# Kernel tuning notes

Measured on AMD Instinct MI355X. Metric: run time of the kernel, lower is better.

The kernel has to match this reference:

```python
import jax, jax.numpy as jnp
import numpy as np

N, E, G = 100000, 1600000, 256
F_IN, HID, NCLS = 16, 64, 2
EPS = 1e-5


def segment_mean(v, seg, num_segments):
    s = jax.ops.segment_sum(v, seg, num_segments=num_segments)
    c = jax.ops.segment_sum(jnp.ones((v.shape[0], 1), v.dtype), seg, num_segments=num_segments)
    return s / jnp.maximum(c, 1.0)


def graph_norm(x, seg, weight, bias, mean_scale):
    # PyG GraphNorm: per-graph mean/var with learnable mean_scale
    mean = segment_mean(x, seg, G)                      # [G, C]
    centered = x - mean_scale * mean[seg]               # [N, C]
    var = segment_mean(centered * centered, seg, G)     # [G, C]
    return weight * centered * jax.lax.rsqrt(var[seg] + EPS) + bias


def gcn_conv(x, W, b, row, col, n):
    # PyG GCNConv: h = x @ W; symmetric norm with added self-loops; scatter-add; + bias
    h = x @ W                                           # [N, C_out]
    deg = jnp.zeros((n,), x.dtype).at[row].add(1.0) + 1.0  # +1 self-loop
    dinv = jax.lax.rsqrt(deg)
    norm = (dinv[row] * dinv[col])[:, None]             # [E, 1]
    agg = jnp.zeros_like(h).at[row].add(norm * h[col])  # neighbor messages
    agg = agg + (dinv * dinv)[:, None] * h              # self-loop messages
    return agg + b


def setup_inputs():
    key = jax.random.key(0)
    ks = jax.random.split(key, 16)
    x = jax.random.normal(ks[0], (N, F_IN), jnp.float32)
    edge_index = jax.random.randint(ks[1], (2, E), 0, N, jnp.int32)
    batch = jnp.sort(jax.random.randint(ks[2], (N,), 0, G, jnp.int32))
    s = lambda k, shp: jax.random.normal(k, shp, jnp.float32) * 0.05
    return {
        "x": x, "edge_index": edge_index, "batch": batch,
        "gn0_w": jnp.ones((F_IN,)), "gn0_b": jnp.zeros((F_IN,)), "gn0_ms": jnp.ones((F_IN,)),
        "W1": s(ks[3], (F_IN, HID)), "b1": jnp.zeros((HID,)),
        "gn1_w": jnp.ones((HID,)), "gn1_b": jnp.zeros((HID,)), "gn1_ms": jnp.ones((HID,)),
        "W2": s(ks[4], (HID, HID)), "b2": jnp.zeros((HID,)),
        "gn2_w": jnp.ones((HID,)), "gn2_b": jnp.zeros((HID,)), "gn2_ms": jnp.ones((HID,)),
        "W3": s(ks[5], (HID, HID)), "b3": jnp.zeros((HID,)),
        "Wd": s(ks[6], (HID, HID)), "bd": jnp.zeros((HID,)),
        "Wo": s(ks[7], (HID, NCLS)), "bo": jnp.zeros((NCLS,)),
    }


def reference(x, edge_index, batch, gn0_w, gn0_b, gn0_ms, W1, b1, gn1_w, gn1_b, gn1_ms,
              W2, b2, gn2_w, gn2_b, gn2_ms, W3, b3, Wd, bd, Wo, bo):
    row, col = edge_index[0], edge_index[1]
    h = graph_norm(x, batch, gn0_w, gn0_b, gn0_ms)
    h = jax.nn.relu(gcn_conv(h, W1, b1, row, col, N))
    h = graph_norm(h, batch, gn1_w, gn1_b, gn1_ms)
    h = jax.nn.relu(gcn_conv(h, W2, b2, row, col, N))
    h = graph_norm(h, batch, gn2_w, gn2_b, gn2_ms)
    h = jax.nn.relu(gcn_conv(h, W3, b3, row, col, N))
    g = segment_mean(h, batch, G)                       # global_mean_pool -> [G, HID]
    # dropout is identity in eval mode
    g = jax.nn.relu(g @ Wd + bd)
    logits = g @ Wo + bo
    return jax.nn.softmax(logits, axis=1)
```

## Files before the change

### kernel.cpp

```cpp
#include <hip/hip_runtime.h>
#include <hip/hip_bf16.h>

#define NN 100000
#define NE 1600000
#define NG 256
#define FIN 16
#define HID 64
#define NBK 391
#define NTILE 391
#define PMAX 4864

__device__ __forceinline__ int lower_bound_i(const int* __restrict__ b, int n, int v) {
    int lo = 0, hi = n;
    while (lo < hi) { int m = (lo + hi) >> 1; if (b[m] < v) lo = m + 1; else hi = m; }
    return lo;
}

__device__ __forceinline__ unsigned pack_bf16(float a, float b) {
    unsigned ua = __float_as_uint(a), ub = __float_as_uint(b);
    ua = (ua + 0x7fffu + ((ua >> 16) & 1u)) >> 16;
    ub = (ub + 0x7fffu + ((ub >> 16) & 1u)) & 0xffff0000u;
    return ua | ub;
}
#define BF_LO(u) __uint_as_float((u) << 16)
#define BF_HI(u) __uint_as_float((u) & 0xffff0000u)

__global__ __launch_bounds__(512) void k_zb(int* __restrict__ bhist) {
    bhist[threadIdx.x] = 0;
}

__global__ __launch_bounds__(512) void k_bhist(const int4* __restrict__ row4, int* __restrict__ bhist) {
    __shared__ int h[NBK];
    for (int i = threadIdx.x; i < NBK; i += 512) h[i] = 0;
    __syncthreads();
    int t0 = blockIdx.x * 1024 + threadIdx.x;
#pragma unroll
    for (int it = 0; it < 2; ++it) {
        int t = t0 + it * 512;
        if (t < NE / 4) {
            int4 r = row4[t];
            atomicAdd(&h[r.x >> 8], 1); atomicAdd(&h[r.y >> 8], 1);
            atomicAdd(&h[r.z >> 8], 1); atomicAdd(&h[r.w >> 8], 1);
        }
    }
    __syncthreads();
    for (int i = threadIdx.x; i < NBK; i += 512)
        if (h[i]) atomicAdd(&bhist[i], h[i]);
}

__global__ __launch_bounds__(512) void k_bscan(const int* __restrict__ bhist, int* __restrict__ bbase,
                                               int* __restrict__ bcur) {
    __shared__ int sc[512];
    int t = threadIdx.x;
    int v = (t < NBK) ? bhist[t] : 0;
    sc[t] = v;
    __syncthreads();
    int acc = v;
    for (int off = 1; off < 512; off <<= 1) {
        int add = (t >= off) ? sc[t - off] : 0;
        __syncthreads();
        acc += add;
        sc[t] = acc;
        __syncthreads();
    }
    if (t < NBK) { bbase[t] = acc - v; bcur[t] = acc - v; }
    if (t == NBK - 1) bbase[NBK] = acc;
}

__global__ __launch_bounds__(512) void k_bscatter(const int4* __restrict__ row4, const int4* __restrict__ col4,
                                                  int* __restrict__ bcur, int2* __restrict__ pairs) {
    __shared__ int lh[NBK], lofs[NBK], lbase[NBK], lc[NBK];
    __shared__ int sc[512];
    __shared__ int2 stg[4096];
    for (int i = threadIdx.x; i < NBK; i += 512) { lh[i] = 0; lc[i] = 0; }
    __syncthreads();
    int t0 = blockIdx.x * 1024 + threadIdx.x;
#pragma unroll
    for (int it = 0; it < 2; ++it) {
        int t = t0 + it * 512;
        if (t < NE / 4) {
            int4 r = row4[t];
            atomicAdd(&lh[r.x >> 8], 1); atomicAdd(&lh[r.y >> 8], 1);
            atomicAdd(&lh[r.z >> 8], 1); atomicAdd(&lh[r.w >> 8], 1);
        }
    }
    __syncthreads();
    {
        int t = threadIdx.x;
        int v = (t < NBK) ? lh[t] : 0;
        sc[t] = v;
        __syncthreads();
        int acc = v;
        for (int off = 1; off < 512; off <<= 1) {
            int add = (t >= off) ? sc[t - off] : 0;
            __syncthreads();
            acc += add;
            sc[t] = acc;
            __syncthreads();
        }
        if (t < NBK) lofs[t] = acc - v;
    }
    if (threadIdx.x < NBK) {
        int c = lh[threadIdx.x];
        lbase[threadIdx.x] = c ? atomicAdd(&bcur[threadIdx.x], c) : 0;
    }
    __syncthreads();
#pragma unroll
    for (int it = 0; it < 2; ++it) {
        int t = t0 + it * 512;
        if (t < NE / 4) {
            int4 r = row4[t];
            int4 c = col4[t];
            int b, rk;
            b = r.x >> 8; rk = atomicAdd(&lc[b], 1); stg[lofs[b] + rk] = make_int2(r.x, c.x);
            b = r.y >> 8; rk = atomicAdd(&lc[b], 1); stg[lofs[b] + rk] = make_int2(r.y, c.y);
            b = r.z >> 8; rk = atomicAdd(&lc[b], 1); stg[lofs[b] + rk] = make_int2(r.z, c.z);
            b = r.w >> 8; rk = atomicAdd(&lc[b], 1); stg[lofs[b] + rk] = make_int2(r.w, c.w);
        }
    }
    __syncthreads();
    int nv = min(4096, NE - blockIdx.x * 4096);
    for (int j = threadIdx.x; j < nv; j += 512) {
        int2 p = stg[j];
        int b = p.x >> 8;
        pairs[lbase[b] + (j - lofs[b])] = p;
    }
}

__global__ __launch_bounds__(256) void k_bsort(const int2* __restrict__ pairs, const int* __restrict__ bbase,
                                               int* __restrict__ csr_col, int* __restrict__ startv,
                                               int* __restrict__ degc, float* __restrict__ dinv) {
    __shared__ int2 prs[PMAX];
    __shared__ int colo[PMAX];
    __shared__ int cnt[256], ofs[256], c2[256], sc[256];
    int b = blockIdx.x;
    int s = bbase[b];
    int n = min(bbase[b + 1] - s, PMAX);
    cnt[threadIdx.x] = 0;
    c2[threadIdx.x] = 0;
    __syncthreads();
    for (int i = threadIdx.x; i < n; i += 256) {
        int2 p = pairs[s + i];
        prs[i] = p;
        atomicAdd(&cnt[p.x & 255], 1);
    }
    __syncthreads();
    {
        int t = threadIdx.x, v = cnt[t];
        sc[t] = v;
        __syncthreads();
        int acc = v;
        for (int off = 1; off < 256; off <<= 1) {
            int add = (t >= off) ? sc[t - off] : 0;
            __syncthreads();
            acc += add;
            sc[t] = acc;
            __syncthreads();
        }
        ofs[t] = acc - v;
    }
    __syncthreads();
    for (int i = threadIdx.x; i < n; i += 256) {
        int2 p = prs[i];
        int lr = p.x & 255;
        int rk = atomicAdd(&c2[lr], 1);
        colo[ofs[lr] + rk] = p.y;
    }
    __syncthreads();
    for (int i = threadIdx.x; i < n; i += 256) csr_col[s + i] = colo[i];
    int r = (b << 8) + threadIdx.x;
    if (r < NN) {
        int c = cnt[threadIdx.x];
        startv[r] = s + ofs[threadIdx.x];
        degc[r] = c;
        dinv[r] = rsqrtf((float)(c + 1));
    }
}

__global__ __launch_bounds__(256) void k_graphnorm16(const float* __restrict__ x, const int* __restrict__ batch,
                              const float* __restrict__ w, const float* __restrict__ b,
                              const float* __restrict__ ms, const float* __restrict__ dinv,
                              unsigned* __restrict__ xb) {
    constexpr int C = FIN, NPB = 256 / C;
    __shared__ float red[NPB][C], red2[NPB][C];
    __shared__ float mm_s[C], rs_s[C];
    int g = blockIdx.x;
    int s = lower_bound_i(batch, NN, g);
    int e = lower_bound_i(batch, NN, g + 1);
    float fc = (float)max(e - s, 1);
    int c = threadIdx.x % C, slot = threadIdx.x / C;

    float a1 = 0.f, a2 = 0.f;
    for (int i = s + slot; i < e; i += NPB) { float v = x[i * C + c]; a1 += v; a2 += v * v; }
    red[slot][c] = a1;
    red2[slot][c] = a2;
    __syncthreads();
    if (threadIdx.x < C) {
        float t1 = 0.f, t2 = 0.f;
        for (int k = 0; k < NPB; k++) { t1 += red[k][threadIdx.x]; t2 += red2[k][threadIdx.x]; }
        float mean = t1 / fc;
        float mm = ms[threadIdx.x] * mean;
        float var = t2 / fc - 2.f * mm * mean + mm * mm;
        mm_s[threadIdx.x] = mm;
        rs_s[threadIdx.x] = rsqrtf(var + 1e-5f);
    }
    __syncthreads();
    float mm = mm_s[c], ww = w[c] * rs_s[c], bb = b[c];
    for (int i = s + slot; i < e; i += NPB) {
        float v = (ww * (x[i * C + c] - mm) + bb) * dinv[i];
        float partner = __shfl_xor(v, 1);
        if ((c & 1) == 0) xb[(long)i * 8 + (c >> 1)] = pack_bf16(v, partner);
    }
}

__global__ __launch_bounds__(256) void k_gnstats(const float* __restrict__ x, const int* __restrict__ batch,
                          const float* __restrict__ w, const float* __restrict__ b,
                          const float* __restrict__ ms,
                          float* __restrict__ tabA, float* __restrict__ tabB) {
    constexpr int C = 64, NPB = 4;
    __shared__ float red[NPB][C], red2[NPB][C];
    int g = blockIdx.x;
    int s = lower_bound_i(batch, NN, g);
    int e = lower_bound_i(batch, NN, g + 1);
    float fc = (float)max(e - s, 1);
    int c = threadIdx.x & 63, slot = threadIdx.x >> 6;

    float a1 = 0.f, a2 = 0.f;
    for (int i = s + slot; i < e; i += NPB) { float v = x[i * C + c]; a1 += v; a2 += v * v; }
    red[slot][c] = a1;
    red2[slot][c] = a2;
    __syncthreads();
    if (threadIdx.x < C) {
        float t1 = 0.f, t2 = 0.f;
        for (int k = 0; k < NPB; k++) { t1 += red[k][threadIdx.x]; t2 += red2[k][threadIdx.x]; }
        float mean = t1 / fc;
        float mm = ms[threadIdx.x] * mean;
        float var = t2 / fc - 2.f * mm * mean + mm * mm;
        float A = w[threadIdx.x] * rsqrtf(var + 1e-5f);
        tabA[g * C + threadIdx.x] = A;
        tabB[g * C + threadIdx.x] = b[threadIdx.x] - A * mm;
    }
}

__global__ __launch_bounds__(256) void k_gg16(const unsigned* __restrict__ xb, const int* __restrict__ startv,
                        const int* __restrict__ degc, const float* __restrict__ dinv,
                        const int* __restrict__ csr_col, const float* __restrict__ W,
                        const float* __restrict__ bias, float* __restrict__ out) {
    __shared__ float Ws[FIN * 64];
    for (int i = threadIdx.x; i < FIN * 64; i += 256) Ws[i] = W[i];
    __syncthreads();
    int wave = (blockIdx.x * blockDim.x + threadIdx.x) >> 6;
    if (wave >= NN) return;
    int lane = threadIdx.x & 63;
    int p = lane & 7, g = lane >> 3;
    int s = startv[wave], cnt = degc[wave];
    float di = dinv[wave];
    float ax = 0.f, ay = 0.f;
    int k = g;
    for (; k + 8 < cnt; k += 16) {
        int c0 = csr_col[s + k], c1 = csr_col[s + k + 8];
        unsigned u0 = xb[(long)c0 * 8 + p], u1 = xb[(long)c1 * 8 + p];
        ax += BF_LO(u0) + BF_LO(u1);
        ay += BF_HI(u0) + BF_HI(u1);
    }
    for (; k < cnt; k += 8) {
        int c0 = csr_col[s + k];
        unsigned u0 = xb[(long)c0 * 8 + p];
        ax += BF_LO(u0);
        ay += BF_HI(u0);
    }
    ax += __shfl_xor(ax, 8);  ay += __shfl_xor(ay, 8);
    ax += __shfl_xor(ax, 16); ay += __shfl_xor(ay, 16);
    ax += __shfl_xor(ax, 32); ay += __shfl_xor(ay, 32);
    if (g == 0) {
        unsigned u = xb[(long)wave * 8 + p];
        ax = (ax + BF_LO(u)) * di;
        ay = (ay + BF_HI(u)) * di;
    }
    int j = lane;
    float acc = bias[j];
#pragma unroll
    for (int kk = 0; kk < 8; kk++) {
        float vx = __shfl(ax, kk);
        float vy = __shfl(ay, kk);
        acc += vx * Ws[(2 * kk) * 64 + j] + vy * Ws[(2 * kk + 1) * 64 + j];
    }
    out[(long)wave * 64 + j] = fmaxf(acc, 0.f);
}

__global__ __launch_bounds__(256) void k_gather64(const unsigned* __restrict__ h2, const int* __restrict__ startv,
                           const int* __restrict__ degc, const float* __restrict__ dinv,
                           const int* __restrict__ csr_col, const float* __restrict__ bias,
                           float* __restrict__ out) {
    int wave = (blockIdx.x * blockDim.x + threadIdx.x) >> 6;
    if (wave >= NN) return;
    int lane = threadIdx.x & 63;
    int p = lane & 31, g = lane >> 5;
    int s = startv[wave], cnt = degc[wave];
    float di = dinv[wave];
    float ax = 0.f, ay = 0.f;
    if (g == 0) {
        unsigned u = h2[(long)wave * 32 + p];
        ax = BF_LO(u);
        ay = BF_HI(u);
    }
    int k = g;
    for (; k + 6 < cnt; k += 8) {
        int c0 = csr_col[s + k], c1 = csr_col[s + k + 2],
            c2 = csr_col[s + k + 4], c3 = csr_col[s + k + 6];
        unsigned u0 = h2[(long)c0 * 32 + p], u1 = h2[(long)c1 * 32 + p],
                 u2 = h2[(long)c2 * 32 + p], u3 = h2[(long)c3 * 32 + p];
        ax += BF_LO(u0) + BF_LO(u1) + BF_LO(u2) + BF_LO(u3);
        ay += BF_HI(u0) + BF_HI(u1) + BF_HI(u2) + BF_HI(u3);
    }
    for (; k < cnt; k += 2) {
        int c0 = csr_col[s + k];
        unsigned u0 = h2[(long)c0 * 32 + p];
        ax += BF_LO(u0);
        ay += BF_HI(u0);
    }
    ax += __shfl_xor(ax, 32);
    ay += __shfl_xor(ay, 32);
    if (g == 0) {
        float2 r;
        r.x = fmaxf(ax * di + bias[2 * p], 0.f);
        r.y = fmaxf(ay * di + bias[2 * p + 1], 0.f);
        ((float2*)out)[(long)wave * 32 + p] = r;
    }
}

__global__ __launch_bounds__(256) void k_gemm64n(const float* __restrict__ x, const int* __restrict__ batch,
                          const float* __restrict__ tabA, const float* __restrict__ tabB,
                          const float* __restrict__ W, const float* __restrict__ dinv,
                          unsigned* __restrict__ h2) {
    constexpr int NPB = 100;
    __shared__ float xs[NPB * 64];
    __shared__ int gb[NPB];
    int base = blockIdx.x * NPB;
    int j = threadIdx.x & 63;
    float w[64];
#pragma unroll
    for (int k = 0; k < 64; k++) w[k] = W[k * 64 + j];
    for (int i = threadIdx.x; i < NPB; i += 256) gb[i] = batch[base + i];
    __syncthreads();
    for (int i = threadIdx.x; i < NPB * 64; i += 256) {
        int node = i >> 6, c = i & 63;
        int g2 = gb[node];
        xs[i] = tabA[g2 * 64 + c] * x[(long)(base + node) * 64 + c] + tabB[g2 * 64 + c];
    }
    __syncthreads();
    int s0 = threadIdx.x >> 6;
    for (int r = 0; r < 25; r++) {
        int sl = s0 * 25 + r;
        const float4* xv = (const float4*)&xs[sl * 64];
        float acc = 0.f;
#pragma unroll
        for (int k4 = 0; k4 < 16; k4++) {
            float4 v = xv[k4];
            acc += v.x * w[4 * k4] + v.y * w[4 * k4 + 1] + v.z * w[4 * k4 + 2] + v.w * w[4 * k4 + 3];
        }
        acc *= dinv[base + sl];
        float part = __shfl_xor(acc, 1);
        if ((j & 1) == 0) h2[(long)(base + sl) * 32 + (j >> 1)] = pack_bf16(acc, part);
    }
}

__global__ __launch_bounds__(1024) void k_pool(const float* __restrict__ x, const int* __restrict__ batch,
                       float* __restrict__ gpool) {
    __shared__ float red[16][64];
    int g = blockIdx.x;
    int s = lower_bound_i(batch, NN, g);
    int e = lower_bound_i(batch, NN, g + 1);
    int c = threadIdx.x & 63, slot = threadIdx.x >> 6;
    float acc = 0.f;
    for (int i = s + slot; i < e; i += 16) acc += x[i * 64 + c];
    red[slot][c] = acc;
    __syncthreads();
    if (threadIdx.x < 64) {
        float t = 0.f;
        for (int k = 0; k < 16; k++) t += red[k][threadIdx.x];
        gpool[g * 64 + threadIdx.x] = t / (float)max(e - s, 1);
    }
}

__global__ __launch_bounds__(64) void k_head(const float* __restrict__ gpool, const float* __restrict__ Wd,
                       const float* __restrict__ bd, const float* __restrict__ Wo,
                       const float* __restrict__ bo, float* __restrict__ out) {
    int g = blockIdx.x, j = threadIdx.x;
    __shared__ float gs[64];
    gs[j] = gpool[g * 64 + j];
    __syncthreads();
    float acc = bd[j];
    for (int k = 0; k < 64; k++) acc += gs[k] * Wd[k * 64 + j];
    float hv = fmaxf(acc, 0.f);
    float p0 = hv * Wo[j * 2 + 0], p1 = hv * Wo[j * 2 + 1];
    for (int off = 32; off; off >>= 1) { p0 += __shfl_down(p0, off); p1 += __shfl_down(p1, off); }
    if (j == 0) {
        float l0 = p0 + bo[0], l1 = p1 + bo[1];
        float m = fmaxf(l0, l1);
        float e0 = expf(l0 - m), e1 = expf(l1 - m);
        float inv = 1.f / (e0 + e1);
        out[g * 2 + 0] = e0 * inv;
        out[g * 2 + 1] = e1 * inv;
    }
}

extern "C" void kernel_launch(void* const* d_in, const int* in_sizes, int n_in,
                              void* d_out, int out_size, void* d_ws, size_t ws_size,
                              hipStream_t stream) {
    const float* x = (const float*)d_in[0];
    const int* ei = (const int*)d_in[1];
    const int* row = ei;
    const int* col = ei + NE;
    const int* batch = (const int*)d_in[2];
    const float* gn0w = (const float*)d_in[3];
    const float* gn0b = (const float*)d_in[4];
    const float* gn0ms = (const float*)d_in[5];
    const float* W1 = (const float*)d_in[6];
    const float* b1 = (const float*)d_in[7];
    const float* gn1w = (const float*)d_in[8];
    const float* gn1b = (const float*)d_in[9];
    const float* gn1ms = (const float*)d_in[10];
    const float* W2 = (const float*)d_in[11];
    const float* b2 = (const float*)d_in[12];
    const float* gn2w = (const float*)d_in[13];
    const float* gn2b = (const float*)d_in[14];
    const float* gn2ms = (const float*)d_in[15];
    const float* W3 = (const float*)d_in[16];
    const float* b3 = (const float*)d_in[17];
    const float* Wd = (const float*)d_in[18];
    const float* bd = (const float*)d_in[19];
    const float* Wo = (const float*)d_in[20];
    const float* bo = (const float*)d_in[21];
    float* outp = (float*)d_out;

    int* bhist = (int*)d_ws;
    int* bbase = bhist + 512;
    int* bcur = bbase + 512;
    int* startv = bcur + 512;
    int* degc = startv + NN;
    float* dinv = (float*)(degc + NN);
    int* csr_col = (int*)(dinv + NN);
    float* bufA = (float*)(csr_col + NE);
    float* bufB = bufA + (long)NN * HID;
    unsigned* h2 = (unsigned*)(bufB + (long)NN * HID);
    unsigned* xb = h2 + (long)NN * 32;
    float* tabA = (float*)(xb + (long)NN * 8);
    float* tabB = tabA + NG * HID;
    float* gpool = tabB + NG * HID;
    int2* pairs = (int2*)bufA;

    k_zb<<<1, 512, 0, stream>>>(bhist);
    k_bhist<<<NTILE, 512, 0, stream>>>((const int4*)row, bhist);
    k_bscan<<<1, 512, 0, stream>>>(bhist, bbase, bcur);
    k_bscatter<<<NTILE, 512, 0, stream>>>((const int4*)row, (const int4*)col, bcur, pairs);
    k_bsort<<<NBK, 256, 0, stream>>>(pairs, bbase, csr_col, startv, degc, dinv);

    k_graphnorm16<<<NG, 256, 0, stream>>>(x, batch, gn0w, gn0b, gn0ms, dinv, xb);
    k_gg16<<<(NN * 64 + 255) / 256, 256, 0, stream>>>(xb, startv, degc, dinv, csr_col, W1, b1, bufA);

    k_gnstats<<<NG, 256, 0, stream>>>(bufA, batch, gn1w, gn1b, gn1ms, tabA, tabB);
    k_gemm64n<<<NN / 100, 256, 0, stream>>>(bufA, batch, tabA, tabB, W2, dinv, h2);
    k_gather64<<<(NN * 64 + 255) / 256, 256, 0, stream>>>(h2, startv, degc, dinv, csr_col, b2, bufB);

    k_gnstats<<<NG, 256, 0, stream>>>(bufB, batch, gn2w, gn2b, gn2ms, tabA, tabB);
    k_gemm64n<<<NN / 100, 256, 0, stream>>>(bufB, batch, tabA, tabB, W3, dinv, h2);
    k_gather64<<<(NN * 64 + 255) / 256, 256, 0, stream>>>(h2, startv, degc, dinv, csr_col, b3, bufA);

    k_pool<<<NG, 1024, 0, stream>>>(bufA, batch, gpool);
    k_head<<<NG, 64, 0, stream>>>(gpool, Wd, bd, Wo, bo, outp);
}
```

Before: 454.9 us.

## Use bf16 MFMA GEMMs with per-graph folded GraphNorm weights and bf16 activations

Replaces the scalar FP32 node GEMMs with bf16 MFMA 16x16x32 kernels that run over per-graph 16-node tiles built by a new tiling kernel. GraphNorm scale and shift are folded into a per-graph weight matrix and bias, computed in the stats kernel. The first layer is split into a 16-wide gather and a separate MFMA GEMM. Intermediate activations are stored as bf16 instead of fp32 to cut memory traffic. In exchange it adds precision loss from bf16 weights and activations, extra launches, and padding waste on partial tiles.

```diff
diff --git a/kernel.cpp b/kernel.cpp
--- a/kernel.cpp
+++ b/kernel.cpp
@@ -9,6 +9,7 @@
 #define NBK 391
 #define NTILE 391
 #define PMAX 4864
+#define MAXT (NN / 16 + NG)
 
 __device__ __forceinline__ int lower_bound_i(const int* __restrict__ b, int n, int v) {
     int lo = 0, hi = n;
@@ -24,6 +25,10 @@
 }
 #define BF_LO(u) __uint_as_float((u) << 16)
 #define BF_HI(u) __uint_as_float((u) & 0xffff0000u)
+
+typedef __attribute__((ext_vector_type(8))) short bf16x8;
+typedef __attribute__((ext_vector_type(4))) float f32x4;
+union FU { uint4 u; bf16x8 v; };
 
 __global__ __launch_bounds__(512) void k_zb(int* __restrict__ bhist) {
     bhist[threadIdx.x] = 0;
@@ -177,6 +182,49 @@
     }
 }
 
+__global__ __launch_bounds__(256) void k_tiles(const int* __restrict__ batch, int* __restrict__ ntot,
+                                               int* __restrict__ tg, int* __restrict__ tbase,
+                                               int* __restrict__ tcnt) {
+    __shared__ int gst[NG + 1];
+    __shared__ int sc[NG];
+    int t = threadIdx.x;
+    gst[t] = lower_bound_i(batch, NN, t);
+    if (t == 0) gst[NG] = NN;
+    __syncthreads();
+    int ng = gst[t + 1] - gst[t];
+    int nt = (ng + 15) >> 4;
+    sc[t] = nt;
+    __syncthreads();
+    int acc = nt;
+    for (int off = 1; off < NG; off <<= 1) {
+        int add = (t >= off) ? sc[t - off] : 0;
+        __syncthreads();
+        acc += add;
+        sc[t] = acc;
+        __syncthreads();
+    }
+    int ofs = acc - nt;
+    for (int i = 0; i < nt; i++) {
+        tg[ofs + i] = t;
+        tbase[ofs + i] = gst[t] + i * 16;
+        tcnt[ofs + i] = min(16, ng - i * 16);
+    }
+    if (t == NG - 1) ntot[0] = acc;
+}
+
+__global__ __launch_bounds__(256) void k_prepw1(const float* __restrict__ W1, unsigned* __restrict__ Wt1p) {
+    int t = threadIdx.x;
+    int j = t >> 2, kq = t & 3;
+#pragma unroll
+    for (int i = 0; i < 4; i++) {
+        int idx = kq * 4 + i;
+        int k = idx * 2;
+        unsigned v = 0;
+        if (k < FIN) v = pack_bf16(W1[k * 64 + j], W1[(k + 1) * 64 + j]);
+        Wt1p[j * 16 + idx] = v;
+    }
+}
+
 __global__ __launch_bounds__(256) void k_graphnorm16(const float* __restrict__ x, const int* __restrict__ batch,
                               const float* __restrict__ w, const float* __restrict__ b,
                               const float* __restrict__ ms, const float* __restrict__ dinv,
@@ -213,12 +261,13 @@
     }
 }
 
-__global__ __launch_bounds__(256) void k_gnstats(const float* __restrict__ x, const int* __restrict__ batch,
+__global__ __launch_bounds__(256) void k_gnstats2(const unsigned* __restrict__ xw, const int* __restrict__ batch,
                           const float* __restrict__ w, const float* __restrict__ b,
-                          const float* __restrict__ ms,
-                          float* __restrict__ tabA, float* __restrict__ tabB) {
+                          const float* __restrict__ ms, const float* __restrict__ W,
+                          unsigned* __restrict__ Wtp, float* __restrict__ bias2) {
     constexpr int C = 64, NPB = 4;
     __shared__ float red[NPB][C], red2[NPB][C];
+    __shared__ float sA[C], sB[C];
     int g = blockIdx.x;
     int s = lower_bound_i(batch, NN, g);
     int e = lower_bound_i(batch, NN, g + 1);
@@ -226,7 +275,11 @@
     int c = threadIdx.x & 63, slot = threadIdx.x >> 6;
 
     float a1 = 0.f, a2 = 0.f;
-    for (int i = s + slot; i < e; i += NPB) { float v = x[i * C + c]; a1 += v; a2 += v * v; }
+    for (int i = s + slot; i < e; i += NPB) {
+        unsigned u = xw[(long)i * 32 + (c >> 1)];
+        float v = (c & 1) ? BF_HI(u) : BF_LO(u);
+        a1 += v; a2 += v * v;
+    }
     red[slot][c] = a1;
     red2[slot][c] = a2;
     __syncthreads();
@@ -237,18 +290,28 @@
         float mm = ms[threadIdx.x] * mean;
         float var = t2 / fc - 2.f * mm * mean + mm * mm;
         float A = w[threadIdx.x] * rsqrtf(var + 1e-5f);
-        tabA[g * C + threadIdx.x] = A;
-        tabB[g * C + threadIdx.x] = b[threadIdx.x] - A * mm;
-    }
-}
-
-__global__ __launch_bounds__(256) void k_gg16(const unsigned* __restrict__ xb, const int* __restrict__ startv,
-                        const int* __restrict__ degc, const float* __restrict__ dinv,
-                        const int* __restrict__ csr_col, const float* __restrict__ W,
-                        const float* __restrict__ bias, float* __restrict__ out) {
-    __shared__ float Ws[FIN * 64];
-    for (int i = threadIdx.x; i < FIN * 64; i += 256) Ws[i] = W[i];
-    __syncthreads();
+        sA[threadIdx.x] = A;
+        sB[threadIdx.x] = b[threadIdx.x] - A * mm;
+    }
+    __syncthreads();
+    int j = threadIdx.x >> 2, kq = threadIdx.x & 3;
+    unsigned* wrow = Wtp + ((long)g * 64 + j) * 32 + kq * 8;
+    float part = 0.f;
+#pragma unroll
+    for (int i = 0; i < 8; i++) {
+        int k = kq * 16 + 2 * i;
+        float w0 = W[k * 64 + j], w1 = W[(k + 1) * 64 + j];
+        wrow[i] = pack_bf16(sA[k] * w0, sA[k + 1] * w1);
+        part += sB[k] * w0 + sB[k + 1] * w1;
+    }
+    part += __shfl_xor(part, 1);
+    part += __shfl_xor(part, 2);
+    if (kq == 0) bias2[g * 64 + j] = part;
+}
+
+__global__ __launch_bounds__(256) void k_gather16(const unsigned* __restrict__ xb, const int* __restrict__ startv,
+                           const int* __restrict__ degc, const float* __restrict__ dinv,
+                           const int* __restrict__ csr_col, unsigned* __restrict__ agg) {
     int wave = (blockIdx.x * blockDim.x + threadIdx.x) >> 6;
     if (wave >= NN) return;
     int lane = threadIdx.x & 63;
@@ -276,22 +339,67 @@
         unsigned u = xb[(long)wave * 8 + p];
         ax = (ax + BF_LO(u)) * di;
         ay = (ay + BF_HI(u)) * di;
-    }
-    int j = lane;
-    float acc = bias[j];
-#pragma unroll
-    for (int kk = 0; kk < 8; kk++) {
-        float vx = __shfl(ax, kk);
-        float vy = __shfl(ay, kk);
-        acc += vx * Ws[(2 * kk) * 64 + j] + vy * Ws[(2 * kk + 1) * 64 + j];
-    }
-    out[(long)wave * 64 + j] = fmaxf(acc, 0.f);
+        agg[(long)wave * 16 + p] = pack_bf16(ax, ay);
+    } else if (g == 1) {
+        agg[(long)wave * 16 + 8 + p] = 0u;
+    }
+}
+
+template <int KU, bool PERG, bool RELU, bool DINV>
+__global__ __launch_bounds__(256) void k_gemmT(const unsigned* __restrict__ Ain, const unsigned* __restrict__ Wt,
+                        const float* __restrict__ biasv, const float* __restrict__ dinv,
+                        const int* __restrict__ ntot, const int* __restrict__ tg,
+                        const int* __restrict__ tbase, const int* __restrict__ tcnt,
+                        unsigned* __restrict__ Aout) {
+    const int RW = KU * 16;
+    int tix = blockIdx.x * 4 + (threadIdx.x >> 6);
+    if (tix >= ntot[0]) return;
+    int g = tg[tix], base = tbase[tix], n = tcnt[tix];
+    int l = threadIdx.x & 63, r = l & 15, q = l >> 4;
+    FU a[KU];
+#pragma unroll
+    for (int s = 0; s < KU; s++) {
+        if (r < n) a[s].u = *(const uint4*)(Ain + (long)(base + r) * RW + s * 16 + q * 4);
+        else a[s].u = make_uint4(0, 0, 0, 0);
+    }
+    const unsigned* wb = PERG ? (Wt + (long)g * 64 * RW) : Wt;
+    f32x4 acc[4];
+#pragma unroll
+    for (int t = 0; t < 4; t++) {
+        acc[t] = (f32x4){0.f, 0.f, 0.f, 0.f};
+#pragma unroll
+        for (int s = 0; s < KU; s++) {
+            FU bfrag;
+            bfrag.u = *(const uint4*)(wb + (long)(t * 16 + r) * RW + s * 16 + q * 4);
+            acc[t] = __builtin_amdgcn_mfma_f32_16x16x32_bf16(a[s].v, bfrag.v, acc[t], 0, 0, 0);
+        }
+    }
+    const float* bb = PERG ? (biasv + g * 64) : biasv;
+    float dv[4];
+#pragma unroll
+    for (int e = 0; e < 4; e++) {
+        int node = base + q * 4 + e;
+        dv[e] = DINV ? ((node < NN) ? dinv[node] : 0.f) : 1.f;
+    }
+#pragma unroll
+    for (int t = 0; t < 4; t++) {
+        float bv = bb[t * 16 + r];
+#pragma unroll
+        for (int e = 0; e < 4; e++) {
+            float v = acc[t][e] + bv;
+            if (RELU) v = fmaxf(v, 0.f);
+            if (DINV) v *= dv[e];
+            float part = __shfl_xor(v, 1);
+            if ((q * 4 + e) < n && (r & 1) == 0)
+                Aout[(long)(base + q * 4 + e) * 32 + t * 8 + (r >> 1)] = pack_bf16(v, part);
+        }
+    }
 }
 
 __global__ __launch_bounds__(256) void k_gather64(const unsigned* __restrict__ h2, const int* __restrict__ startv,
                            const int* __restrict__ degc, const float* __restrict__ dinv,
                            const int* __restrict__ csr_col, const float* __restrict__ bias,
-                           float* __restrict__ out) {
+                           unsigned* __restrict__ outp) {
     int wave = (blockIdx.x * blockDim.x + threadIdx.x) >> 6;
     if (wave >= NN) return;
     int lane = threadIdx.x & 63;
@@ -322,50 +430,13 @@
     ax += __shfl_xor(ax, 32);
     ay += __shfl_xor(ay, 32);
     if (g == 0) {
-        float2 r;
-        r.x = fmaxf(ax * di + bias[2 * p], 0.f);
-        r.y = fmaxf(ay * di + bias[2 * p + 1], 0.f);
-        ((float2*)out)[(long)wave * 32 + p] = r;
-    }
-}
-
-__global__ __launch_bounds__(256) void k_gemm64n(const float* __restrict__ x, const int* __restrict__ batch,
-                          const float* __restrict__ tabA, const float* __restrict__ tabB,
-                          const float* __restrict__ W, const float* __restrict__ dinv,
-                          unsigned* __restrict__ h2) {
-    constexpr int NPB = 100;
-    __shared__ float xs[NPB * 64];
-    __shared__ int gb[NPB];
-    int base = blockIdx.x * NPB;
-    int j = threadIdx.x & 63;
-    float w[64];
-#pragma unroll
-    for (int k = 0; k < 64; k++) w[k] = W[k * 64 + j];
-    for (int i = threadIdx.x; i < NPB; i += 256) gb[i] = batch[base + i];
-    __syncthreads();
-    for (int i = threadIdx.x; i < NPB * 64; i += 256) {
-        int node = i >> 6, c = i & 63;
-        int g2 = gb[node];
-        xs[i] = tabA[g2 * 64 + c] * x[(long)(base + node) * 64 + c] + tabB[g2 * 64 + c];
-    }
-    __syncthreads();
-    int s0 = threadIdx.x >> 6;
-    for (int r = 0; r < 25; r++) {
-        int sl = s0 * 25 + r;
-        const float4* xv = (const float4*)&xs[sl * 64];
-        float acc = 0.f;
-#pragma unroll
-        for (int k4 = 0; k4 < 16; k4++) {
-            float4 v = xv[k4];
-            acc += v.x * w[4 * k4] + v.y * w[4 * k4 + 1] + v.z * w[4 * k4 + 2] + v.w * w[4 * k4 + 3];
-        }
-        acc *= dinv[base + sl];
-        float part = __shfl_xor(acc, 1);
-        if ((j & 1) == 0) h2[(long)(base + sl) * 32 + (j >> 1)] = pack_bf16(acc, part);
-    }
-}
-
-__global__ __launch_bounds__(1024) void k_pool(const float* __restrict__ x, const int* __restrict__ batch,
+        float vx = fmaxf(ax * di + bias[2 * p], 0.f);
+        float vy = fmaxf(ay * di + bias[2 * p + 1], 0.f);
+        outp[(long)wave * 32 + p] = pack_bf16(vx, vy);
+    }
+}
+
+__global__ __launch_bounds__(1024) void k_pool(const unsigned* __restrict__ xw, const int* __restrict__ batch,
                        float* __restrict__ gpool) {
     __shared__ float red[16][64];
     int g = blockIdx.x;
@@ -373,7 +444,10 @@
     int e = lower_bound_i(batch, NN, g + 1);
     int c = threadIdx.x & 63, slot = threadIdx.x >> 6;
     float acc = 0.f;
-    for (int i = s + slot; i < e; i += 16) acc += x[i * 64 + c];
+    for (int i = s + slot; i < e; i += 16) {
+        unsigned u = xw[(long)i * 32 + (c >> 1)];
+        acc += (c & 1) ? BF_HI(u) : BF_LO(u);
+    }
     red[slot][c] = acc;
     __syncthreads();
     if (threadIdx.x < 64) {
@@ -441,14 +515,22 @@
     int* degc = startv + NN;
     float* dinv = (float*)(degc + NN);
     int* csr_col = (int*)(dinv + NN);
-    float* bufA = (float*)(csr_col + NE);
-    float* bufB = bufA + (long)NN * HID;
-    unsigned* h2 = (unsigned*)(bufB + (long)NN * HID);
-    unsigned* xb = h2 + (long)NN * 32;
-    float* tabA = (float*)(xb + (long)NN * 8);
-    float* tabB = tabA + NG * HID;
-    float* gpool = tabB + NG * HID;
+    int* ntot = csr_col + NE;
+    int* tg = ntot + 16;
+    int* tbase = tg + 6608;
+    int* tcnt = tbase + 6608;
+    unsigned* Wt1p = (unsigned*)(tcnt + 6608);
+    unsigned* Wtp = Wt1p + 1024;
+    float* bias2 = (float*)(Wtp + (long)NG * 64 * 32);
+    unsigned* xb = (unsigned*)(bias2 + NG * 64);
+    unsigned* agg16 = xb + (long)NN * 8;
+    unsigned* bufA = agg16 + (long)NN * 16;
+    unsigned* bufB = bufA + (long)NN * 32;
+    unsigned* h2 = bufB + (long)NN * 32;
+    float* gpool = (float*)(h2 + (long)NN * 32);
     int2* pairs = (int2*)bufA;
+
+    const int NBG = (MAXT + 3) / 4;
 
     k_zb<<<1, 512, 0, stream>>>(bhist);
     k_bhist<<<NTILE, 512, 0, stream>>>((const int4*)row, bhist);
@@ -456,15 +538,19 @@
     k_bscatter<<<NTILE, 512, 0, stream>>>((const int4*)row, (const int4*)col, bcur, pairs);
     k_bsort<<<NBK, 256, 0, stream>>>(pairs, bbase, csr_col, startv, degc, dinv);
 
+    k_tiles<<<1, 256, 0, stream>>>(batch, ntot, tg, tbase, tcnt);
+    k_prepw1<<<1, 256, 0, stream>>>(W1, Wt1p);
+
     k_graphnorm16<<<NG, 256, 0, stream>>>(x, batch, gn0w, gn0b, gn0ms, dinv, xb);
-    k_gg16<<<(NN * 64 + 255) / 256, 256, 0, stream>>>(xb, startv, degc, dinv, csr_col, W1, b1, bufA);
-
-    k_gnstats<<<NG, 256, 0, stream>>>(bufA, batch, gn1w, gn1b, gn1ms, tabA, tabB);
-    k_gemm64n<<<NN / 100, 256, 0, stream>>>(bufA, batch, tabA, tabB, W2, dinv, h2);
+    k_gather16<<<(NN * 64 + 255) / 256, 256, 0, stream>>>(xb, startv, degc, dinv, csr_col, agg16);
+    k_gemmT<1, false, true, false><<<NBG, 256, 0, stream>>>(agg16, Wt1p, b1, dinv, ntot, tg, tbase, tcnt, bufA);
+
+    k_gnstats2<<<NG, 256, 0, stream>>>(bufA, batch, gn1w, gn1b, gn1ms, W2, Wtp, bias2);
+    k_gemmT<2, true, false, true><<<NBG, 256, 0, stream>>>(bufA, Wtp, bias2, dinv, ntot, tg, tbase, tcnt, h2);
     k_gather64<<<(NN * 64 + 255) / 256, 256, 0, stream>>>(h2, startv, degc, dinv, csr_col, b2, bufB);
 
-    k_gnstats<<<NG, 256, 0, stream>>>(bufB, batch, gn2w, gn2b, gn2ms, tabA, tabB);
-    k_gemm64n<<<NN / 100, 256, 0, stream>>>(bufB, batch, tabA, tabB, W3, dinv, h2);
+    k_gnstats2<<<NG, 256, 0, stream>>>(bufB, batch, gn2w, gn2b, gn2ms, W3, Wtp, bias2);
+    k_gemmT<2, true, false, true><<<NBG, 256, 0, stream>>>(bufB, Wtp, bias2, dinv, ntot, tg, tbase, tcnt, h2);
     k_gather64<<<(NN * 64 + 255) / 256, 256, 0, stream>>>(h2, startv, degc, dinv, csr_col, b3, bufA);
 
     k_pool<<<NG, 1024, 0, stream>>>(bufA, batch, gpool);
```

New measurement: 440.5 us. 1.03x faster.
